# Kernel tuning notes

Measured on AMD Instinct MI355X. Metric: run time of the kernel, lower is better.

Reference implementation:

```python
import jax, jax.numpy as jnp
import numpy as np

DIM = 512
HEADS = 8
DH = DIM // HEADS
SCALE = DH ** -0.5
LN_EPS = 1e-5


def setup_inputs() -> dict:
    key = jax.random.key(0)
    ks = jax.random.split(key, 6)
    b, n = 16, 1024
    x = jax.random.normal(ks[0], (b, n, DIM), dtype=jnp.float32)
    # to_qkv: Linear(dim, 3*dim, bias=False)
    Wqkv = jax.random.normal(ks[1], (DIM, 3 * DIM), dtype=jnp.float32) * (DIM ** -0.5)
    # LayerNorm(inner_dim) affine params
    ln_g = jnp.ones((DIM,), dtype=jnp.float32)
    ln_b = jnp.zeros((DIM,), dtype=jnp.float32)
    # to_out: Linear(inner_dim, dim) with bias
    Wo = jax.random.normal(ks[2], (DIM, DIM), dtype=jnp.float32) * (DIM ** -0.5)
    bo = jnp.zeros((DIM,), dtype=jnp.float32)
    return {"x": x, "Wqkv": Wqkv, "ln_g": ln_g, "ln_b": ln_b, "Wo": Wo, "bo": bo}


def reference(x, Wqkv, ln_g, ln_b, Wo, bo):
    b, n, d = x.shape
    h, dh = HEADS, DH
    qkv = x @ Wqkv                              # [b, n, 3d]
    q, k, v = jnp.split(qkv, 3, axis=-1)        # each [b, n, d]
    def to_heads(t):
        return t.reshape(b, n, h, dh).transpose(0, 2, 1, 3)  # [b, h, n, dh]
    q, k, v = to_heads(q), to_heads(k), to_heads(v)
    dots = jnp.einsum('bhid,bhjd->bhij', q, k) * SCALE       # [b, h, n, n]
    attn = jax.nn.relu(dots)                                 # ReLU instead of softmax
    out = jnp.einsum('bhij,bhjd->bhid', attn, v)             # [b, h, n, dh]
    out = out.transpose(0, 2, 1, 3).reshape(b, n, d)         # [b, n, d]
    # LayerNorm over last dim
    mu = jnp.mean(out, axis=-1, keepdims=True)
    var = jnp.var(out, axis=-1, keepdims=True)
    out = (out - mu) * jax.lax.rsqrt(var + LN_EPS) * ln_g + ln_b
    return out @ Wo + bo
```

## Files before the change

kernel.cpp:

```cpp
#include <hip/hip_runtime.h>
#include <cstdint>
#include <cstddef>

typedef unsigned short u16;
typedef float f32x4 __attribute__((ext_vector_type(4)));
typedef short short8 __attribute__((ext_vector_type(8)));
typedef u16 u16x4 __attribute__((ext_vector_type(4)));
typedef unsigned u32x2 __attribute__((ext_vector_type(2)));

#define MFMA_BF16(acc, a, b) \
  asm("v_mfma_f32_16x16x32_bf16 %0, %1, %2, %0" : "+v"(acc) : "v"(a), "v"(b))

#define CVT_PK(w, lo, hi) \
  asm("v_cvt_pk_bf16_f32 %0, %1, %2" : "=v"(w) : "v"(lo), "v"(hi))

#define GLDS16(gp, lp) __builtin_amdgcn_global_load_lds( \
    (__attribute__((address_space(1))) void*)(void*)(uintptr_t)(gp), \
    (__attribute__((address_space(3))) void*)(lp), 16, 0, 0)

static __device__ __forceinline__ u16 f2bf(float f) {
  union { float f; unsigned u; } x; x.f = f;
  unsigned u = x.u + 0x7fffu + ((x.u >> 16) & 1u);
  return (u16)(u >> 16);
}

__global__ __launch_bounds__(256) void prep_kernel(const float* __restrict__ x,
                                                   u16* __restrict__ xbf,
                                                   const float* __restrict__ Wqkv,
                                                   u16* __restrict__ wqkvt,
                                                   const float* __restrict__ Wo,
                                                   u16* __restrict__ wot) {
  __shared__ float tile[64][65];
  const int bid = blockIdx.x, tid = threadIdx.x;
  if (bid < 4096) {
    for (int i = bid * 256 + tid; i < 2097152; i += 4096 * 256) {
      f32x4 v = ((const f32x4*)x)[i];
      u16x4 o;
      o[0] = f2bf(v[0]); o[1] = f2bf(v[1]); o[2] = f2bf(v[2]); o[3] = f2bf(v[3]);
      ((u16x4*)xbf)[i] = o;
    }
    return;
  }
  const float* src; u16* dst; int R, C, sclim, bx, by;
  if (bid < 4288) {
    int t = bid - 4096; bx = t % 24; by = t / 24;
    src = Wqkv; dst = wqkvt; R = 512; C = 1536; sclim = 512;
  } else {
    int t = bid - 4288; bx = t & 7; by = t >> 3;
    src = Wo; dst = wot; R = 512; C = 512; sclim = 0;
  }
  int c0 = bx * 64, r0 = by * 64;
  for (int t = tid; t < 4096; t += 256) {
    int r = t >> 6, c = t & 63;
    tile[r][c] = src[(size_t)(r0 + r) * C + c0 + c];
  }
  __syncthreads();
  for (int t = tid; t < 4096; t += 256) {
    int rr = t >> 6, cc = t & 63;
    float sc = (c0 + rr) < sclim ? 0.125f : 1.0f;
    dst[(size_t)(c0 + rr) * R + r0 + cc] = f2bf(tile[cc][rr] * sc);
  }
}

__global__ __launch_bounds__(256) void gemm_qkv_kernel(const u16* __restrict__ A,
                                                       const u16* __restrict__ BT,
                                                       u16* __restrict__ qk,
                                                       u16* __restrict__ vT) {
  __shared__ u16 smem[16896];
  u16* As = smem;
  u16* Bs = smem + 8192;
  const int tid = threadIdx.x, lane = tid & 63, wave = tid >> 6;
  const int wr = wave >> 1, wc = wave & 1;
  const int bid = blockIdx.x;
  const int lin = (bid & 7) * 192 + (bid >> 3);
  const int my = lin / 12, nx = lin - my * 12;
  const int m0 = my * 128, n0 = nx * 128;
  f32x4 acc[4][4] = {};
  for (int kt = 0; kt < 8; ++kt) {
    int k0 = kt * 64;
    __syncthreads();
    #pragma unroll
    for (int t = 0; t < 4; ++t) {
      int ch = wave * 4 + t;
      GLDS16(A + (size_t)(m0 + ch * 8 + (lane >> 3)) * 512 + k0 + (lane & 7) * 8, &As[ch * 512]);
      GLDS16(BT + (size_t)(n0 + ch * 8 + (lane >> 3)) * 512 + k0 + (lane & 7) * 8, &Bs[ch * 512]);
    }
    __syncthreads();
    #pragma unroll
    for (int kk = 0; kk < 2; ++kk) {
      short8 af[4], bfr[4];
      #pragma unroll
      for (int m = 0; m < 4; ++m)
        af[m] = *(const short8*)&As[(wr * 64 + m * 16 + (lane & 15)) * 64 + kk * 32 + (lane >> 4) * 8];
      #pragma unroll
      for (int n = 0; n < 4; ++n)
        bfr[n] = *(const short8*)&Bs[(wc * 64 + n * 16 + (lane & 15)) * 64 + kk * 32 + (lane >> 4) * 8];
      #pragma unroll
      for (int m = 0; m < 4; ++m)
        #pragma unroll
        for (int n = 0; n < 4; ++n)
          MFMA_BF16(acc[m][n], af[m], bfr[n]);
    }
  }
  const int row0 = m0 + wr * 64, col0 = n0 + wc * 64;
  if (n0 < 1024) {
    #pragma unroll
    for (int m = 0; m < 4; ++m) {
      int row = row0 + m * 16 + (lane >> 4) * 4;
      #pragma unroll
      for (int n = 0; n < 4; ++n) {
        int col = col0 + n * 16 + (lane & 15);
        unsigned w0, w1;
        CVT_PK(w0, acc[m][n][0], acc[m][n][1]);
        CVT_PK(w1, acc[m][n][2], acc[m][n][3]);
        qk[(size_t)(row + 0) * 1024 + col] = (u16)(w0 & 0xffffu);
        qk[(size_t)(row + 1) * 1024 + col] = (u16)(w0 >> 16);
        qk[(size_t)(row + 2) * 1024 + col] = (u16)(w1 & 0xffffu);
        qk[(size_t)(row + 3) * 1024 + col] = (u16)(w1 >> 16);
      }
    }
  } else {
    __syncthreads();
    const int lo = lane & 15, g = lane >> 4;
    #pragma unroll
    for (int m = 0; m < 4; ++m) {
      int tl0 = wr * 64 + m * 16 + g * 4;
      #pragma unroll
      for (int n = 0; n < 4; ++n) {
        int dl = wc * 64 + n * 16 + lo;
        u32x2 pk2;
        CVT_PK(pk2[0], acc[m][n][0], acc[m][n][1]);
        CVT_PK(pk2[1], acc[m][n][2], acc[m][n][3]);
        *(u32x2*)&smem[dl * 132 + tl0] = pk2;
      }
    }
    __syncthreads();
    const int bb = m0 >> 10, nn0 = m0 & 1023, d0 = n0 - 1024;
    for (int t = tid; t < 128 * 32; t += 256) {
      int d = t >> 5, sg = t & 31;
      u16x4 v = *(const u16x4*)&smem[d * 132 + sg * 4];
      *(u16x4*)&vT[(size_t)(bb * 512 + d0 + d) * 1024 + nn0 + sg * 4] = v;
    }
  }
}

__global__ __launch_bounds__(256) void attn_kernel(const u16* __restrict__ qk,
                                                   const u16* __restrict__ vT,
                                                   u16* __restrict__ aout) {
  __shared__ u16 smem[32768];
  u16* Ks = smem;
  u16* Vs = smem + 8192;
  u16* Ss = smem + 16384;
  const int tid = threadIdx.x, lane = tid & 63, wave = tid >> 6;
  const int wr = wave >> 1, wc = wave & 1;
  const int L = blockIdx.x;
  const int qt2 = L >> 7, bh = L & 127, h = bh & 7, b = bh >> 3;
  const size_t qrow0 = (size_t)b * 1024 + qt2 * 256;

  short8 qf[2][4][2];
  #pragma unroll
  for (int q = 0; q < 2; ++q)
    #pragma unroll
    for (int m = 0; m < 4; ++m)
      #pragma unroll
      for (int kk = 0; kk < 2; ++kk)
        qf[q][m][kk] = *(const short8*)&qk[(qrow0 + q * 128 + wr * 64 + m * 16 + (lane & 15)) * 1024
                                           + h * 64 + kk * 32 + (lane >> 4) * 8];
  f32x4 acc[2][4][2] = {};
  for (int jt = 0; jt < 8; ++jt) {
    __syncthreads();
    const u16* Kg = qk + ((size_t)b * 1024 + jt * 128) * 1024 + 512 + h * 64;
    const u16* Vg = vT + ((size_t)b * 512 + h * 64) * 1024 + jt * 128;
    #pragma unroll
    for (int t = 0; t < 4; ++t) {
      int ch = wave * 4 + t;
      GLDS16(Kg + (size_t)(ch * 8 + (lane >> 3)) * 1024 + ((lane & 7) ^ (lane >> 3)) * 8,
             &Ks[ch * 512]);
      GLDS16(Vg + (size_t)(ch * 4 + (lane >> 4)) * 1024 + ((lane & 15) ^ (t * 4 + (lane >> 4))) * 8,
             &Vs[ch * 512]);
    }
    __syncthreads();
    #pragma unroll
    for (int q = 0; q < 2; ++q) {
      f32x4 sacc[4][4] = {};
      __builtin_amdgcn_s_setprio(1);
      #pragma unroll
      for (int kk = 0; kk < 2; ++kk) {
        short8 kf[4];
        #pragma unroll
        for (int n = 0; n < 4; ++n) {
          int r = wc * 64 + n * 16 + (lane & 15);
          int slot = kk * 4 + (lane >> 4);
          kf[n] = *(const short8*)&Ks[r * 64 + ((slot ^ (r & 7)) * 8)];
        }
        #pragma unroll
        for (int n = 0; n < 4; ++n)
          #pragma unroll
          for (int m = 0; m < 4; ++m)
            MFMA_BF16(sacc[n][m], kf[n], qf[q][m][kk]);
      }
      __builtin_amdgcn_s_setprio(0);
      if (q == 1) __syncthreads();
      #pragma unroll
      for (int m = 0; m < 4; ++m) {
        int i = wr * 64 + m * 16 + (lane & 15);
        unsigned rowbase = (unsigned)i * 256;
        unsigned sw = (unsigned)(i & 15) << 4;
        #pragma unroll
        for (int n = 0; n < 4; ++n) {
          int j0 = wc * 64 + n * 16 + (lane >> 4) * 4;
          float a0 = fmaxf(sacc[n][m][0], 0.f), a1 = fmaxf(sacc[n][m][1], 0.f);
          float a2 = fmaxf(sacc[n][m][2], 0.f), a3 = fmaxf(sacc[n][m][3], 0.f);
          u32x2 pk2;
          CVT_PK(pk2[0], a0, a1);
          CVT_PK(pk2[1], a2, a3);
          *(u32x2*)((char*)Ss + (rowbase + (((unsigned)j0 * 2) ^ sw))) = pk2;
        }
      }
      __syncthreads();
      __builtin_amdgcn_s_setprio(1);
      #pragma unroll
      for (int ks = 0; ks < 4; ++ks) {
        short8 sa[4], vb[2];
        #pragma unroll
        for (int m = 0; m < 4; ++m) {
          int i = wr * 64 + m * 16 + (lane & 15);
          unsigned c2 = (unsigned)(ks * 32 + (lane >> 4) * 8) * 2;
          sa[m] = *(const short8*)((const char*)Ss + (unsigned)i * 256 + (c2 ^ ((unsigned)(i & 15) << 4)));
        }
        #pragma unroll
        for (int n = 0; n < 2; ++n) {
          int r = wc * 32 + n * 16 + (lane & 15);
          int slot = ks * 4 + (lane >> 4);
          vb[n] = *(const short8*)&Vs[r * 128 + ((slot ^ (r & 15)) * 8)];
        }
        #pragma unroll
        for (int m = 0; m < 4; ++m)
          #pragma unroll
          for (int n = 0; n < 2; ++n)
            MFMA_BF16(acc[q][m][n], sa[m], vb[n]);
      }
      __builtin_amdgcn_s_setprio(0);
    }
  }
  #pragma unroll
  for (int q = 0; q < 2; ++q)
    #pragma unroll
    for (int m = 0; m < 4; ++m) {
      int row = q * 128 + wr * 64 + m * 16 + (lane >> 4) * 4;
      #pragma unroll
      for (int n = 0; n < 2; ++n) {
        int col = h * 64 + wc * 32 + n * 16 + (lane & 15);
        unsigned w0, w1;
        CVT_PK(w0, acc[q][m][n][0], acc[q][m][n][1]);
        CVT_PK(w1, acc[q][m][n][2], acc[q][m][n][3]);
        aout[(qrow0 + row + 0) * 512 + col] = (u16)(w0 & 0xffffu);
        aout[(qrow0 + row + 1) * 512 + col] = (u16)(w0 >> 16);
        aout[(qrow0 + row + 2) * 512 + col] = (u16)(w1 & 0xffffu);
        aout[(qrow0 + row + 3) * 512 + col] = (u16)(w1 >> 16);
      }
    }
}

__global__ __launch_bounds__(256) void ln_kernel(const u16* __restrict__ x,
                                                 const float* __restrict__ g,
                                                 const float* __restrict__ bt,
                                                 u16* __restrict__ y) {
  const int lane = threadIdx.x & 63, wave = threadIdx.x >> 6;
  const size_t row = (size_t)blockIdx.x * 4 + wave;
  const u16* xr = x + row * 512;
  u16x4 h0 = *(const u16x4*)&xr[lane * 8];
  u16x4 h1 = *(const u16x4*)&xr[lane * 8 + 4];
  float v[8];
  #pragma unroll
  for (int i = 0; i < 4; ++i) {
    union { unsigned u; float f; } a, bu;
    a.u = (unsigned)h0[i] << 16;  v[i] = a.f;
    bu.u = (unsigned)h1[i] << 16; v[4 + i] = bu.f;
  }
  float s = 0.f, q = 0.f;
  #pragma unroll
  for (int i = 0; i < 8; ++i) { s += v[i]; q += v[i] * v[i]; }
  #pragma unroll
  for (int o = 32; o > 0; o >>= 1) { s += __shfl_xor(s, o); q += __shfl_xor(q, o); }
  float mean = s * (1.f / 512.f);
  float var  = q * (1.f / 512.f) - mean * mean;
  float rstd = rsqrtf(var + 1e-5f);
  f32x4 g0 = *(const f32x4*)&g[lane * 8],  g1 = *(const f32x4*)&g[lane * 8 + 4];
  f32x4 b0 = *(const f32x4*)&bt[lane * 8], b1 = *(const f32x4*)&bt[lane * 8 + 4];
  u16x4 o0, o1;
  #pragma unroll
  for (int i = 0; i < 4; ++i) {
    o0[i] = f2bf((v[i] - mean) * rstd * g0[i] + b0[i]);
    o1[i] = f2bf((v[4 + i] - mean) * rstd * g1[i] + b1[i]);
  }
  *(u16x4*)&y[row * 512 + lane * 8] = o0;
  *(u16x4*)&y[row * 512 + lane * 8 + 4] = o1;
}

__global__ __launch_bounds__(256) void gemm_out_kernel(const u16* __restrict__ A,
                                                       const u16* __restrict__ BT,
                                                       const float* __restrict__ bias,
                                                       float* __restrict__ out) {
  __shared__ u16 As[128 * 64];
  __shared__ u16 Bs[128 * 64];
  const int tid = threadIdx.x, lane = tid & 63, wave = tid >> 6;
  const int wr = wave >> 1, wc = wave & 1;
  const int bid = blockIdx.x;
  const int lin = (bid & 7) * 64 + (bid >> 3);
  const int m0 = (lin >> 2) * 128, n0 = (lin & 3) * 128;
  f32x4 acc[4][4] = {};
  for (int kt = 0; kt < 8; ++kt) {
    int k0 = kt * 64;
    __syncthreads();
    #pragma unroll
    for (int t = 0; t < 4; ++t) {
      int ch = wave * 4 + t;
      GLDS16(A + (size_t)(m0 + ch * 8 + (lane >> 3)) * 512 + k0 + (lane & 7) * 8, &As[ch * 512]);
      GLDS16(BT + (size_t)(n0 + ch * 8 + (lane >> 3)) * 512 + k0 + (lane & 7) * 8, &Bs[ch * 512]);
    }
    __syncthreads();
    #pragma unroll
    for (int kk = 0; kk < 2; ++kk) {
      short8 af[4], bfr[4];
      #pragma unroll
      for (int m = 0; m < 4; ++m)
        af[m] = *(const short8*)&As[(wr * 64 + m * 16 + (lane & 15)) * 64 + kk * 32 + (lane >> 4) * 8];
      #pragma unroll
      for (int n = 0; n < 4; ++n)
        bfr[n] = *(const short8*)&Bs[(wc * 64 + n * 16 + (lane & 15)) * 64 + kk * 32 + (lane >> 4) * 8];
      #pragma unroll
      for (int m = 0; m < 4; ++m)
        #pragma unroll
        for (int n = 0; n < 4; ++n)
          MFMA_BF16(acc[m][n], af[m], bfr[n]);
    }
  }
  const int row0 = m0 + wr * 64, col0 = n0 + wc * 64;
  #pragma unroll
  for (int m = 0; m < 4; ++m) {
    int row = row0 + m * 16 + (lane >> 4) * 4;
    #pragma unroll
    for (int n = 0; n < 4; ++n) {
      int col = col0 + n * 16 + (lane & 15);
      float bv = bias[col];
      #pragma unroll
      for (int i = 0; i < 4; ++i)
        out[(size_t)(row + i) * 512 + col] = acc[m][n][i] + bv;
    }
  }
}

extern "C" void kernel_launch(void* const* d_in, const int* in_sizes, int n_in,
                              void* d_out, int out_size, void* d_ws, size_t ws_size,
                              hipStream_t stream) {
  const float* x    = (const float*)d_in[0];
  const float* Wqkv = (const float*)d_in[1];
  const float* ln_g = (const float*)d_in[2];
  const float* ln_b = (const float*)d_in[3];
  const float* Wo   = (const float*)d_in[4];
  const float* bo   = (const float*)d_in[5];
  float* out = (float*)d_out;
  char* ws = (char*)d_ws;

  u16*   xbf   = (u16*)(ws);
  u16*   wqkvt = (u16*)(ws + 16777216);
  u16*   wot   = (u16*)(ws + 18350080);
  u16*   qkb   = (u16*)(ws + 18874368);
  u16*   vtb   = (u16*)(ws + 52428800);
  u16*   att   = (u16*)(ws + 69206016);

  prep_kernel<<<4352, 256, 0, stream>>>(x, xbf, Wqkv, wqkvt, Wo, wot);
  gemm_qkv_kernel<<<1536, 256, 0, stream>>>(xbf, wqkvt, qkb, vtb);
  attn_kernel<<<512, 256, 0, stream>>>(qkb, vtb, att);
  ln_kernel<<<4096, 256, 0, stream>>>(att, ln_g, ln_b, xbf);
  gemm_out_kernel<<<512, 256, 0, stream>>>(xbf, wot, bo, out);
}
```

Baseline: 116.4 us.

## Fold LayerNorm into output GEMM epilogue via precomputed weight sums

Removes the separate LayerNorm kernel by scaling Wo rows by gamma during prep and precomputing per-column sums of gamma*Wo and beta*Wo+bias. The output GEMM computes per-row mean and rstd from the attention output in a prologue and applies them in the epilogue. This avoids writing and re-reading the normalized activations and one launch, at the cost of an extra row read per block and a slow serial reduction in two prep blocks.

Result: slower. 156.0 us (+34.0%).

```diff
diff --git a/kernel.cpp b/kernel.cpp
--- a/kernel.cpp
+++ b/kernel.cpp
@@ -23,13 +23,21 @@
   unsigned u = x.u + 0x7fffu + ((x.u >> 16) & 1u);
   return (u16)(u >> 16);
 }
+static __device__ __forceinline__ float bf2f(u16 h) {
+  union { unsigned u; float f; } x; x.u = (unsigned)h << 16; return x.f;
+}
 
 __global__ __launch_bounds__(256) void prep_kernel(const float* __restrict__ x,
                                                    u16* __restrict__ xbf,
                                                    const float* __restrict__ Wqkv,
                                                    u16* __restrict__ wqkvt,
                                                    const float* __restrict__ Wo,
-                                                   u16* __restrict__ wot) {
+                                                   u16* __restrict__ wgt,
+                                                   const float* __restrict__ g,
+                                                   const float* __restrict__ bvec,
+                                                   const float* __restrict__ bo,
+                                                   float* __restrict__ Sg,
+                                                   float* __restrict__ c2) {
   __shared__ float tile[64][65];
   const int bid = blockIdx.x, tid = threadIdx.x;
   if (bid < 4096) {
@@ -41,24 +49,45 @@
     }
     return;
   }
-  const float* src; u16* dst; int R, C, sclim, bx, by;
   if (bid < 4288) {
-    int t = bid - 4096; bx = t % 24; by = t / 24;
-    src = Wqkv; dst = wqkvt; R = 512; C = 1536; sclim = 512;
-  } else {
-    int t = bid - 4288; bx = t & 7; by = t >> 3;
-    src = Wo; dst = wot; R = 512; C = 512; sclim = 0;
-  }
-  int c0 = bx * 64, r0 = by * 64;
-  for (int t = tid; t < 4096; t += 256) {
-    int r = t >> 6, c = t & 63;
-    tile[r][c] = src[(size_t)(r0 + r) * C + c0 + c];
-  }
-  __syncthreads();
-  for (int t = tid; t < 4096; t += 256) {
-    int rr = t >> 6, cc = t & 63;
-    float sc = (c0 + rr) < sclim ? 0.125f : 1.0f;
-    dst[(size_t)(c0 + rr) * R + r0 + cc] = f2bf(tile[cc][rr] * sc);
+    int t = bid - 4096; int bx = t % 24, by = t / 24;
+    int c0 = bx * 64, r0 = by * 64;
+    for (int t2 = tid; t2 < 4096; t2 += 256) {
+      int r = t2 >> 6, c = t2 & 63;
+      tile[r][c] = Wqkv[(size_t)(r0 + r) * 1536 + c0 + c];
+    }
+    __syncthreads();
+    for (int t2 = tid; t2 < 4096; t2 += 256) {
+      int rr = t2 >> 6, cc = t2 & 63;
+      float sc = (c0 + rr) < 512 ? 0.125f : 1.0f;
+      wqkvt[(size_t)(c0 + rr) * 512 + r0 + cc] = f2bf(tile[cc][rr] * sc);
+    }
+    return;
+  }
+  if (bid < 4352) {
+    int t = bid - 4288; int bx = t & 7, by = t >> 3;
+    int c0 = bx * 64, r0 = by * 64;
+    for (int t2 = tid; t2 < 4096; t2 += 256) {
+      int r = t2 >> 6, c = t2 & 63;
+      tile[r][c] = Wo[(size_t)(r0 + r) * 512 + c0 + c];
+    }
+    __syncthreads();
+    for (int t2 = tid; t2 < 4096; t2 += 256) {
+      int rr = t2 >> 6, cc = t2 & 63;
+      wgt[(size_t)(c0 + rr) * 512 + r0 + cc] = f2bf(tile[cc][rr] * g[r0 + cc]);
+    }
+    return;
+  }
+  {
+    int j = (bid - 4352) * 256 + tid;
+    float sg = 0.f, cc = 0.f;
+    for (int k = 0; k < 512; ++k) {
+      float w = Wo[(size_t)k * 512 + j];
+      sg += bf2f(f2bf(g[k] * w));
+      cc += bvec[k] * w;
+    }
+    Sg[j] = sg;
+    c2[j] = cc + bo[j];
   }
 }
 
@@ -225,8 +254,8 @@
         #pragma unroll
         for (int m = 0; m < 4; ++m) {
           int i = wr * 64 + m * 16 + (lane & 15);
-          unsigned c2 = (unsigned)(ks * 32 + (lane >> 4) * 8) * 2;
-          sa[m] = *(const short8*)((const char*)Ss + (unsigned)i * 256 + (c2 ^ ((unsigned)(i & 15) << 4)));
+          unsigned c2v = (unsigned)(ks * 32 + (lane >> 4) * 8) * 2;
+          sa[m] = *(const short8*)((const char*)Ss + (unsigned)i * 256 + (c2v ^ ((unsigned)(i & 15) << 4)));
         }
         #pragma unroll
         for (int n = 0; n < 2; ++n) {
@@ -262,53 +291,42 @@
     }
 }
 
-__global__ __launch_bounds__(256) void ln_kernel(const u16* __restrict__ x,
-                                                 const float* __restrict__ g,
-                                                 const float* __restrict__ bt,
-                                                 u16* __restrict__ y) {
-  const int lane = threadIdx.x & 63, wave = threadIdx.x >> 6;
-  const size_t row = (size_t)blockIdx.x * 4 + wave;
-  const u16* xr = x + row * 512;
-  u16x4 h0 = *(const u16x4*)&xr[lane * 8];
-  u16x4 h1 = *(const u16x4*)&xr[lane * 8 + 4];
-  float v[8];
-  #pragma unroll
-  for (int i = 0; i < 4; ++i) {
-    union { unsigned u; float f; } a, bu;
-    a.u = (unsigned)h0[i] << 16;  v[i] = a.f;
-    bu.u = (unsigned)h1[i] << 16; v[4 + i] = bu.f;
-  }
-  float s = 0.f, q = 0.f;
-  #pragma unroll
-  for (int i = 0; i < 8; ++i) { s += v[i]; q += v[i] * v[i]; }
-  #pragma unroll
-  for (int o = 32; o > 0; o >>= 1) { s += __shfl_xor(s, o); q += __shfl_xor(q, o); }
-  float mean = s * (1.f / 512.f);
-  float var  = q * (1.f / 512.f) - mean * mean;
-  float rstd = rsqrtf(var + 1e-5f);
-  f32x4 g0 = *(const f32x4*)&g[lane * 8],  g1 = *(const f32x4*)&g[lane * 8 + 4];
-  f32x4 b0 = *(const f32x4*)&bt[lane * 8], b1 = *(const f32x4*)&bt[lane * 8 + 4];
-  u16x4 o0, o1;
-  #pragma unroll
-  for (int i = 0; i < 4; ++i) {
-    o0[i] = f2bf((v[i] - mean) * rstd * g0[i] + b0[i]);
-    o1[i] = f2bf((v[4 + i] - mean) * rstd * g1[i] + b1[i]);
-  }
-  *(u16x4*)&y[row * 512 + lane * 8] = o0;
-  *(u16x4*)&y[row * 512 + lane * 8 + 4] = o1;
-}
-
-__global__ __launch_bounds__(256) void gemm_out_kernel(const u16* __restrict__ A,
+__global__ __launch_bounds__(256) void gemm_out_kernel(const u16* __restrict__ att,
                                                        const u16* __restrict__ BT,
-                                                       const float* __restrict__ bias,
+                                                       const float* __restrict__ Sg,
+                                                       const float* __restrict__ c2,
                                                        float* __restrict__ out) {
-  __shared__ u16 As[128 * 64];
-  __shared__ u16 Bs[128 * 64];
+  __shared__ u16 smem[16896];
+  u16* As = smem;
+  u16* Bs = smem + 8192;
+  float* muL = (float*)&smem[16384];
+  float* rsL = (float*)&smem[16640];
   const int tid = threadIdx.x, lane = tid & 63, wave = tid >> 6;
   const int wr = wave >> 1, wc = wave & 1;
   const int bid = blockIdx.x;
   const int lin = (bid & 7) * 64 + (bid >> 3);
   const int m0 = (lin >> 2) * 128, n0 = (lin & 3) * 128;
+  {
+    const int r = tid >> 1, half = tid & 1;
+    const u16* ar = att + (size_t)(m0 + r) * 512 + half * 256;
+    float s = 0.f, q = 0.f;
+    #pragma unroll
+    for (int i = 0; i < 32; ++i) {
+      short8 hv = *(const short8*)&ar[i * 8];
+      #pragma unroll
+      for (int e = 0; e < 8; ++e) {
+        float f = bf2f((u16)hv[e]);
+        s += f; q += f * f;
+      }
+    }
+    s += __shfl_xor(s, 1); q += __shfl_xor(q, 1);
+    if (half == 0) {
+      float mean = s * (1.f / 512.f);
+      float var  = q * (1.f / 512.f) - mean * mean;
+      muL[r] = mean;
+      rsL[r] = rsqrtf(var + 1e-5f);
+    }
+  }
   f32x4 acc[4][4] = {};
   for (int kt = 0; kt < 8; ++kt) {
     int k0 = kt * 64;
@@ -316,7 +334,7 @@
     #pragma unroll
     for (int t = 0; t < 4; ++t) {
       int ch = wave * 4 + t;
-      GLDS16(A + (size_t)(m0 + ch * 8 + (lane >> 3)) * 512 + k0 + (lane & 7) * 8, &As[ch * 512]);
+      GLDS16(att + (size_t)(m0 + ch * 8 + (lane >> 3)) * 512 + k0 + (lane & 7) * 8, &As[ch * 512]);
       GLDS16(BT + (size_t)(n0 + ch * 8 + (lane >> 3)) * 512 + k0 + (lane & 7) * 8, &Bs[ch * 512]);
     }
     __syncthreads();
@@ -336,17 +354,19 @@
           MFMA_BF16(acc[m][n], af[m], bfr[n]);
     }
   }
-  const int row0 = m0 + wr * 64, col0 = n0 + wc * 64;
+  const int col0 = n0 + wc * 64;
   #pragma unroll
   for (int m = 0; m < 4; ++m) {
-    int row = row0 + m * 16 + (lane >> 4) * 4;
+    int rl = wr * 64 + m * 16 + (lane >> 4) * 4;
+    f32x4 muv = *(const f32x4*)&muL[rl];
+    f32x4 rsv = *(const f32x4*)&rsL[rl];
     #pragma unroll
     for (int n = 0; n < 4; ++n) {
       int col = col0 + n * 16 + (lane & 15);
-      float bv = bias[col];
+      float sg = Sg[col], cc = c2[col];
       #pragma unroll
       for (int i = 0; i < 4; ++i)
-        out[(size_t)(row + i) * 512 + col] = acc[m][n][i] + bv;
+        out[(size_t)(m0 + rl + i) * 512 + col] = rsv[i] * (acc[m][n][i] - muv[i] * sg) + cc;
     }
   }
 }
@@ -365,14 +385,16 @@
 
   u16*   xbf   = (u16*)(ws);
   u16*   wqkvt = (u16*)(ws + 16777216);
-  u16*   wot   = (u16*)(ws + 18350080);
+  u16*   wgt   = (u16*)(ws + 18350080);
   u16*   qkb   = (u16*)(ws + 18874368);
   u16*   vtb   = (u16*)(ws + 52428800);
   u16*   att   = (u16*)(ws + 69206016);
-
-  prep_kernel<<<4352, 256, 0, stream>>>(x, xbf, Wqkv, wqkvt, Wo, wot);
+  float* Sg    = (float*)(ws + 85983232);
+  float* c2    = (float*)(ws + 85985280);
+
+  prep_kernel<<<4354, 256, 0, stream>>>(x, xbf, Wqkv, wqkvt, Wo, wgt,
+                                        ln_g, ln_b, bo, Sg, c2);
   gemm_qkv_kernel<<<1536, 256, 0, stream>>>(xbf, wqkvt, qkb, vtb);
   attn_kernel<<<512, 256, 0, stream>>>(qkb, vtb, att);
-  ln_kernel<<<4096, 256, 0, stream>>>(att, ln_g, ln_b, xbf);
-  gemm_out_kernel<<<512, 256, 0, stream>>>(xbf, wot, bo, out);
-}
+  gemm_out_kernel<<<512, 256, 0, stream>>>(att, wgt, Sg, c2, out);
+}
```
